# Kernel optimization log

Hardware: AMD Instinct MI355X
Metric: run time of the kernel (lower is better)

Reference implementation:

```python
import jax, jax.numpy as jnp
import numpy as np

DIM = 256
NUM_HEADS = 8
HEAD_DIM = DIM // NUM_HEADS
SCALE = HEAD_DIM ** (-0.5)


def setup_inputs() -> dict:
    key = jax.random.key(0)
    k1, k2, k3, k4 = jax.random.split(key, 4)
    x = jax.random.normal(k1, (4, 1, DIM, 12, 12, 12), dtype=jnp.float32)
    w_qkv = jax.random.normal(k2, (3 * DIM, DIM), dtype=jnp.float32) * 0.02
    w_proj = jax.random.normal(k3, (DIM, DIM), dtype=jnp.float32) * 0.02
    b_proj = jax.random.normal(k4, (DIM,), dtype=jnp.float32) * 0.02
    return {"x": x, "w_qkv": w_qkv, "w_proj": w_proj, "b_proj": b_proj}


def reference(x, w_qkv, w_proj, b_proj):
    # x: [P=4, B, C, H, W, D]; 1x1x1 Conv3d == channel matmul
    P, B, C, H, W, D = x.shape
    N = H * W * D
    xf = x.reshape(P, B, C, N)                       # [P,B,C,N]
    qkv = jnp.einsum('pbcn,oc->pbon', xf, w_qkv)     # [P,B,3C,N]
    q, k, v = jnp.split(qkv, 3, axis=2)              # each [P,B,C,N]
    # fold batch*heads
    def heads(t):
        return t.reshape(P, B * NUM_HEADS, HEAD_DIM, N)
    q, k, v = heads(q) * SCALE, heads(k), heads(v)
    attn = jnp.einsum('phcm,phcn->phmn', q, k)       # [P,BH,N,N]
    attn = jax.nn.softmax(attn, axis=-1)
    out = jnp.einsum('phmn,phcn->phcm', attn, v)     # [P,BH,hd,N]
    out = out.reshape(P, B, C, N)
    out = jnp.einsum('pbcn,oc->pbon', out, w_proj) + b_proj[None, None, :, None]
    return out.reshape(P, B, C, H, W, D)
```

## Files before the change

### kernel.cpp

```cpp
#include <hip/hip_runtime.h>

#define NP 4
#define NH 8
#define HD 32
#define CD 256
#define NN 1728
#define NT_TILES 27
#define SCALE_Q2 (0.17677669529663687f * 1.4426950408889634f)

typedef __bf16 bf16x8 __attribute__((ext_vector_type(8)));
typedef __bf16 bf16x4_t __attribute__((ext_vector_type(4)));
typedef short short4_t __attribute__((ext_vector_type(4)));
typedef float f32x4 __attribute__((ext_vector_type(4)));
typedef unsigned short ushort4_t __attribute__((ext_vector_type(4)));
typedef unsigned short ushort8_t __attribute__((ext_vector_type(8)));

__device__ __forceinline__ unsigned short f2bf(float f) {
  unsigned int v = __builtin_bit_cast(unsigned int, f);
  unsigned int r = (v + 0x7FFFu + ((v >> 16) & 1u)) >> 16;
  return (unsigned short)r;
}

__global__ void k_prep(const float* __restrict__ x, unsigned short* __restrict__ xt,
                       const float* __restrict__ wqkv, const float* __restrict__ wproj,
                       unsigned short* __restrict__ wq_b, unsigned short* __restrict__ wp_b) {
  __shared__ __attribute__((aligned(16))) unsigned short tile[64 * 40];
  int bid = blockIdx.x;
  int t = threadIdx.x;
  if (bid >= 864) {
    int idx = ((bid - 864) * 256 + t) * 4;
    const float* src;
    unsigned short* dst;
    if (idx < 196608) { src = wqkv + idx; dst = wq_b + idx; }
    else { src = wproj + (idx - 196608); dst = wp_b + (idx - 196608); }
    float4 v = *(const float4*)src;
    ushort4_t o;
    o[0] = f2bf(v.x); o[1] = f2bf(v.y); o[2] = f2bf(v.z); o[3] = f2bf(v.w);
    *(ushort4_t*)dst = o;
    return;
  }
  int nb = (bid % 27) * 64, cb = ((bid / 27) & 7) * 32, p = bid / 216;
  {
    int c = t >> 3, ch = t & 7;
    const float* src = x + ((size_t)p * CD + cb + c) * NN + nb + ch * 8;
    float4 v0 = *(const float4*)src;
    float4 v1 = *(const float4*)(src + 4);
    int base = ch * 8;
    tile[(base + 0) * 40 + c] = f2bf(v0.x);
    tile[(base + 1) * 40 + c] = f2bf(v0.y);
    tile[(base + 2) * 40 + c] = f2bf(v0.z);
    tile[(base + 3) * 40 + c] = f2bf(v0.w);
    tile[(base + 4) * 40 + c] = f2bf(v1.x);
    tile[(base + 5) * 40 + c] = f2bf(v1.y);
    tile[(base + 6) * 40 + c] = f2bf(v1.z);
    tile[(base + 7) * 40 + c] = f2bf(v1.w);
  }
  __syncthreads();
  {
    int n = t >> 2, ch = t & 3;
    *(ushort8_t*)(xt + ((size_t)p * NN + nb + n) * CD + cb + ch * 8) =
        *(const ushort8_t*)&tile[n * 40 + ch * 8];
  }
}

__global__ void k_qkv(const unsigned short* __restrict__ xt,
                      const unsigned short* __restrict__ wqkv,
                      unsigned short* __restrict__ Qt, unsigned short* __restrict__ Kt,
                      unsigned short* __restrict__ Vv) {
  int p = blockIdx.z, ot = blockIdx.y, nt = blockIdx.x;
  int tid = threadIdx.x, w = tid >> 6, lane = tid & 63, l15 = lane & 15, g = lane >> 4;
  int nbase = nt * 64 + w * 16;
  f32x4 acc[4] = {};
  const unsigned short* arow = xt + ((size_t)p * NN + nbase + l15) * CD + g * 8;
  const unsigned short* wrow = wqkv + ((size_t)(ot * 64 + l15)) * CD + g * 8;
  for (int ks = 0; ks < 8; ks++) {
    bf16x8 a = *(const bf16x8*)(arow + ks * 32);
#pragma unroll
    for (int ob = 0; ob < 4; ob++) {
      bf16x8 b = *(const bf16x8*)(wrow + ob * 16 * CD + ks * 32);
      acc[ob] = __builtin_amdgcn_mfma_f32_16x16x32_bf16(a, b, acc[ob], 0, 0, 0);
    }
  }
#pragma unroll
  for (int ob = 0; ob < 4; ob++) {
    int o = ot * 64 + ob * 16 + l15;
    int wq = o >> 8, rem = o & 255, h = rem >> 5, cc = rem & 31;
    int ph = p * NH + h;
    int nrow = nbase + g * 4;
    if (wq == 0) {
      for (int r = 0; r < 4; r++)
        Qt[((size_t)ph * NN + nrow + r) * HD + cc] = f2bf(acc[ob][r] * SCALE_Q2);
    } else if (wq == 1) {
      for (int r = 0; r < 4; r++)
        Kt[((size_t)ph * NN + nrow + r) * HD + cc] = f2bf(acc[ob][r]);
    } else {
      ushort4_t vs;
      for (int r = 0; r < 4; r++) vs[r] = f2bf(acc[ob][r]);
      *(ushort4_t*)(Vv + ((size_t)ph * HD + cc) * NN + nrow) = vs;
    }
  }
}

__global__ __launch_bounds__(256) void k_attn(const unsigned short* __restrict__ Qt,
                                              const unsigned short* __restrict__ Kt,
                                              const unsigned short* __restrict__ Vv,
                                              unsigned short* __restrict__ Ot) {
  __shared__ __attribute__((aligned(16))) unsigned char lds[2 * (5120 + 4096)];
  int tid = threadIdx.x, w = tid >> 6, lane = tid & 63, l15 = lane & 15, g = lane >> 4;
  int mt = blockIdx.x, ph = blockIdx.y;
  const unsigned short* qptr = Qt + ((size_t)ph * NN + mt * 64 + w * 16 + l15) * HD + g * 8;
  bf16x8 qfrag = *(const bf16x8*)qptr;
  const unsigned short* ktb = Kt + (size_t)ph * NN * HD;
  const unsigned short* vb = Vv + (size_t)ph * HD * NN;
  f32x4 lsum = {0.f, 0.f, 0.f, 0.f};
  f32x4 oacc[2] = {};
  int snl = tid >> 2, sch = tid & 3;
  int svc = tid >> 3, svch = tid & 7;
  const int kst_off = snl * 80 + sch * 16;
  const int vst_off = (svc * 128 + svch * 16) ^ ((svc & 7) << 4);
  f32x4 zacc = {0.f, 0.f, 0.f, 0.f};
  {
    ushort8_t kr = *(const ushort8_t*)(ktb + (size_t)snl * HD + sch * 8);
    ushort8_t vr = *(const ushort8_t*)(vb + (size_t)svc * NN + svch * 8);
    *(ushort8_t*)(lds + kst_off) = kr;
    *(ushort8_t*)(lds + 5120 + vst_off) = vr;
  }
  __syncthreads();
  for (int nt = 0; nt < NT_TILES; nt++) {
    unsigned char* kbuf = lds + (nt & 1) * 9216;
    unsigned char* vbuf = kbuf + 5120;
    unsigned char* kbufN = lds + ((nt + 1) & 1) * 9216;
    unsigned char* vbufN = kbufN + 5120;
    ushort8_t kr, vr;
    bool pre = (nt + 1 < NT_TILES);
    if (pre) {
      kr = *(const ushort8_t*)(ktb + ((size_t)((nt + 1) * 64 + snl)) * HD + sch * 8);
      vr = *(const ushort8_t*)(vb + (size_t)svc * NN + (nt + 1) * 64 + svch * 8);
    }
    f32x4 s[4];
#pragma unroll
    for (int nf = 0; nf < 4; nf++) {
      bf16x8 kb = *(const bf16x8*)(kbuf + (nf * 16 + l15) * 80 + g * 16);
      s[nf] = __builtin_amdgcn_mfma_f32_16x16x32_bf16(kb, qfrag, zacc, 0, 0, 0);
    }
    short4_t pa[4];
#pragma unroll
    for (int nf = 0; nf < 4; nf++) {
      f32x4 e;
#pragma unroll
      for (int r = 0; r < 4; r++) e[r] = __builtin_amdgcn_exp2f(s[nf][r]);
      lsum += e;
      bf16x4_t t;
#pragma unroll
      for (int r = 0; r < 4; r++) t[r] = (__bf16)e[r];
      pa[nf] = __builtin_bit_cast(short4_t, t);
    }
#pragma unroll
    for (int nf = 0; nf < 4; nf++) {
#pragma unroll
      for (int cb = 0; cb < 2; cb++) {
        int c = cb * 16 + l15;
        ushort4_t vq = *(const ushort4_t*)(vbuf + ((c * 128 + nf * 32 + g * 8) ^ ((c & 7) << 4)));
        short4_t va = __builtin_bit_cast(short4_t, vq);
        oacc[cb] = __builtin_amdgcn_mfma_f32_16x16x16bf16_1k(va, pa[nf], oacc[cb], 0, 0, 0);
      }
    }
    if (pre) {
      *(ushort8_t*)(kbufN + kst_off) = kr;
      *(ushort8_t*)(vbufN + vst_off) = vr;
    }
    __syncthreads();
  }
  float total = lsum[0] + lsum[1] + lsum[2] + lsum[3];
  total += __shfl_xor(total, 16);
  total += __shfl_xor(total, 32);
  float inv = 1.0f / total;
  int h = ph & 7, p4 = ph >> 3;
  int m = mt * 64 + w * 16 + l15;
#pragma unroll
  for (int cb = 0; cb < 2; cb++) {
    ushort4_t vs;
#pragma unroll
    for (int rr = 0; rr < 4; rr++) vs[rr] = f2bf(oacc[cb][rr] * inv);
    *(ushort4_t*)(Ot + ((size_t)p4 * NN + m) * CD + h * HD + cb * 16 + g * 4) = vs;
  }
}

__global__ void k_proj(const unsigned short* __restrict__ Ot,
                       const unsigned short* __restrict__ wproj,
                       const float* __restrict__ bproj,
                       float* __restrict__ out) {
  int p = blockIdx.z, ot = blockIdx.y, nt = blockIdx.x;
  int tid = threadIdx.x, w = tid >> 6, lane = tid & 63, l15 = lane & 15, g = lane >> 4;
  int nbase = nt * 64 + w * 16;
  f32x4 acc[4] = {};
  const unsigned short* arow = Ot + ((size_t)p * NN + nbase + l15) * CD + g * 8;
  const unsigned short* wrow = wproj + ((size_t)(ot * 64 + l15)) * CD + g * 8;
  for (int ks = 0; ks < 8; ks++) {
    bf16x8 a = *(const bf16x8*)(arow + ks * 32);
#pragma unroll
    for (int ob = 0; ob < 4; ob++) {
      bf16x8 b = *(const bf16x8*)(wrow + ob * 16 * CD + ks * 32);
      acc[ob] = __builtin_amdgcn_mfma_f32_16x16x32_bf16(a, b, acc[ob], 0, 0, 0);
    }
  }
#pragma unroll
  for (int ob = 0; ob < 4; ob++) {
    int o = ot * 64 + ob * 16 + l15;
    float bias = bproj[o];
    int nrow = nbase + g * 4;
    float4 vs;
    vs.x = acc[ob][0] + bias;
    vs.y = acc[ob][1] + bias;
    vs.z = acc[ob][2] + bias;
    vs.w = acc[ob][3] + bias;
    *(float4*)(out + (size_t)p * CD * NN + (size_t)o * NN + nrow) = vs;
  }
}

extern "C" void kernel_launch(void* const* d_in, const int* in_sizes, int n_in,
                              void* d_out, int out_size, void* d_ws, size_t ws_size,
                              hipStream_t stream) {
  const float* x = (const float*)d_in[0];
  const float* wqkv = (const float*)d_in[1];
  const float* wproj = (const float*)d_in[2];
  const float* bproj = (const float*)d_in[3];
  float* out = (float*)d_out;
  unsigned short* ws = (unsigned short*)d_ws;
  const size_t SZ = (size_t)NP * NN * CD;
  unsigned short* xt = ws;
  unsigned short* Qt = ws + SZ;
  unsigned short* Kt = ws + 2 * SZ;
  unsigned short* Vv = ws + 3 * SZ;
  unsigned short* Ot = ws + 4 * SZ;
  unsigned short* wq_b = ws + 5 * SZ;
  unsigned short* wp_b = ws + 5 * SZ + 196608;
  hipLaunchKernelGGL(k_prep, dim3(1120), dim3(256), 0, stream, x, xt, wqkv, wproj, wq_b, wp_b);
  hipLaunchKernelGGL(k_qkv, dim3(27, 12, NP), dim3(256), 0, stream, xt, wq_b, Qt, Kt, Vv);
  hipLaunchKernelGGL(k_attn, dim3(27, 32), dim3(256), 0, stream, Qt, Kt, Vv, Ot);
  hipLaunchKernelGGL(k_proj, dim3(27, 4, NP), dim3(256), 0, stream, Ot, wp_b, bproj, out);
}
```

Before: 83.53 us.

## Split attention KV range across two blocks and combine partial outputs

Splits the attention loop over key tiles into two halves using a third grid dimension, doubling the block count from 864 to 1728 to better fill the GPU. Each half writes unnormalized bf16 partial outputs and row sums, and a new combine kernel sums them, normalizes, and writes the head-interleaved layout. Because no running max is kept, the partials add directly without rescaling. The cost is an extra kernel launch, extra global traffic, and an additional bf16 rounding of the partials, with workspace reused (xt and the output buffer) as scratch.

```diff
diff --git a/kernel.cpp b/kernel.cpp
--- a/kernel.cpp
+++ b/kernel.cpp
@@ -15,6 +15,10 @@
 typedef unsigned short ushort4_t __attribute__((ext_vector_type(4)));
 typedef unsigned short ushort8_t __attribute__((ext_vector_type(8)));
 
+__device__ __forceinline__ float bf2f(unsigned short u) {
+  unsigned int v = ((unsigned int)u) << 16;
+  return __builtin_bit_cast(float, v);
+}
 __device__ __forceinline__ unsigned short f2bf(float f) {
   unsigned int v = __builtin_bit_cast(unsigned int, f);
   unsigned int r = (v + 0x7FFFu + ((v >> 16) & 1u)) >> 16;
@@ -104,10 +108,13 @@
 __global__ __launch_bounds__(256) void k_attn(const unsigned short* __restrict__ Qt,
                                               const unsigned short* __restrict__ Kt,
                                               const unsigned short* __restrict__ Vv,
-                                              unsigned short* __restrict__ Ot) {
+                                              unsigned short* __restrict__ op0,
+                                              unsigned short* __restrict__ op1,
+                                              float* __restrict__ Lp) {
   __shared__ __attribute__((aligned(16))) unsigned char lds[2 * (5120 + 4096)];
   int tid = threadIdx.x, w = tid >> 6, lane = tid & 63, l15 = lane & 15, g = lane >> 4;
-  int mt = blockIdx.x, ph = blockIdx.y;
+  int mt = blockIdx.x, ph = blockIdx.y, z = blockIdx.z;
+  int t0 = z * 14, tEnd = z ? NT_TILES : 14;
   const unsigned short* qptr = Qt + ((size_t)ph * NN + mt * 64 + w * 16 + l15) * HD + g * 8;
   bf16x8 qfrag = *(const bf16x8*)qptr;
   const unsigned short* ktb = Kt + (size_t)ph * NN * HD;
@@ -120,19 +127,19 @@
   const int vst_off = (svc * 128 + svch * 16) ^ ((svc & 7) << 4);
   f32x4 zacc = {0.f, 0.f, 0.f, 0.f};
   {
-    ushort8_t kr = *(const ushort8_t*)(ktb + (size_t)snl * HD + sch * 8);
-    ushort8_t vr = *(const ushort8_t*)(vb + (size_t)svc * NN + svch * 8);
+    ushort8_t kr = *(const ushort8_t*)(ktb + ((size_t)(t0 * 64 + snl)) * HD + sch * 8);
+    ushort8_t vr = *(const ushort8_t*)(vb + (size_t)svc * NN + t0 * 64 + svch * 8);
     *(ushort8_t*)(lds + kst_off) = kr;
     *(ushort8_t*)(lds + 5120 + vst_off) = vr;
   }
   __syncthreads();
-  for (int nt = 0; nt < NT_TILES; nt++) {
+  for (int nt = t0; nt < tEnd; nt++) {
     unsigned char* kbuf = lds + (nt & 1) * 9216;
     unsigned char* vbuf = kbuf + 5120;
     unsigned char* kbufN = lds + ((nt + 1) & 1) * 9216;
     unsigned char* vbufN = kbufN + 5120;
     ushort8_t kr, vr;
-    bool pre = (nt + 1 < NT_TILES);
+    bool pre = (nt + 1 < tEnd);
     if (pre) {
       kr = *(const ushort8_t*)(ktb + ((size_t)((nt + 1) * 64 + snl)) * HD + sch * 8);
       vr = *(const ushort8_t*)(vb + (size_t)svc * NN + (nt + 1) * 64 + svch * 8);
@@ -174,16 +181,35 @@
   float total = lsum[0] + lsum[1] + lsum[2] + lsum[3];
   total += __shfl_xor(total, 16);
   total += __shfl_xor(total, 32);
-  float inv = 1.0f / total;
-  int h = ph & 7, p4 = ph >> 3;
   int m = mt * 64 + w * 16 + l15;
+  unsigned short* op = z ? op1 : op0;
+  if (g == 0) Lp[(size_t)z * 32 * NN + (size_t)ph * NN + m] = total;
 #pragma unroll
   for (int cb = 0; cb < 2; cb++) {
     ushort4_t vs;
 #pragma unroll
-    for (int rr = 0; rr < 4; rr++) vs[rr] = f2bf(oacc[cb][rr] * inv);
-    *(ushort4_t*)(Ot + ((size_t)p4 * NN + m) * CD + h * HD + cb * 16 + g * 4) = vs;
-  }
+    for (int rr = 0; rr < 4; rr++) vs[rr] = f2bf(oacc[cb][rr]);
+    *(ushort4_t*)(op + ((size_t)ph * NN + m) * 32 + cb * 16 + g * 4) = vs;
+  }
+}
+
+__global__ void k_combine(const unsigned short* __restrict__ op0,
+                          const unsigned short* __restrict__ op1,
+                          const float* __restrict__ Lp,
+                          unsigned short* __restrict__ Ot) {
+  size_t e = ((size_t)blockIdx.x * 256 + threadIdx.x) * 8;
+  size_t r = e >> 5;
+  int c8 = (int)(e & 31);
+  float L = Lp[r] + Lp[(size_t)32 * NN + r];
+  float inv = 1.0f / L;
+  ushort8_t a0 = *(const ushort8_t*)(op0 + e);
+  ushort8_t a1 = *(const ushort8_t*)(op1 + e);
+  ushort8_t o;
+#pragma unroll
+  for (int j = 0; j < 8; j++) o[j] = f2bf((bf2f(a0[j]) + bf2f(a1[j])) * inv);
+  int ph = (int)(r / NN), n = (int)(r % NN);
+  int p = ph >> 3, h = ph & 7;
+  *(ushort8_t*)(Ot + ((size_t)p * NN + n) * CD + h * HD + c8) = o;
 }
 
 __global__ void k_proj(const unsigned short* __restrict__ Ot,
@@ -235,8 +261,12 @@
   unsigned short* Ot = ws + 4 * SZ;
   unsigned short* wq_b = ws + 5 * SZ;
   unsigned short* wp_b = ws + 5 * SZ + 196608;
+  float* Lp = (float*)(ws + 5 * SZ + 262144);
+  unsigned short* op0 = xt;
+  unsigned short* op1 = (unsigned short*)d_out;
   hipLaunchKernelGGL(k_prep, dim3(1120), dim3(256), 0, stream, x, xt, wqkv, wproj, wq_b, wp_b);
   hipLaunchKernelGGL(k_qkv, dim3(27, 12, NP), dim3(256), 0, stream, xt, wq_b, Qt, Kt, Vv);
-  hipLaunchKernelGGL(k_attn, dim3(27, 32), dim3(256), 0, stream, Qt, Kt, Vv, Ot);
+  hipLaunchKernelGGL(k_attn, dim3(27, 32, 2), dim3(256), 0, stream, Qt, Kt, Vv, op0, op1, Lp);
+  hipLaunchKernelGGL(k_combine, dim3(864), dim3(256), 0, stream, op0, op1, Lp, Ot);
   hipLaunchKernelGGL(k_proj, dim3(27, 4, NP), dim3(256), 0, stream, Ot, wp_b, bproj, out);
 }
```

Result: no change. 83.33 us (-0.2%).
